# Performance work log

Measured on AMD Instinct MI355X. Metric: run time of the kernel, lower is better.

The kernel has to match this reference:

```python
import jax, jax.numpy as jnp
import numpy as np

K = 5  # adder 'conv' kernel size
PAD = 2  # same padding


def adder2d(x, w):
    """AdderNet L1-distance convolution: out[b,o,i,j] = -sum_{c,kh,kw} |patch - w|.
    x: [B, C, H, W], w: [O, C, K, K] -> [B, O, H, W]
    """
    O = w.shape[0]
    # im2col patches: [B, C*K*K, H, W]
    patches = jax.lax.conv_general_dilated_patches(
        x, (K, K), (1, 1), [(PAD, PAD), (PAD, PAD)])
    wf = w.reshape(O, -1)  # [O, C*K*K]

    def per_out_channel(wo):
        # sequential over O keeps peak memory at one [B, C*K*K, H, W] temp
        return jnp.abs(patches - wo[None, :, None, None]).sum(axis=1)

    out = jax.lax.map(per_out_channel, wf)  # [O, B, H, W]
    return -jnp.transpose(out, (1, 0, 2, 3))


def prelu(x, a):
    # nn.PReLU with a single shared parameter
    return jnp.where(x >= 0, x, a * x)


def maxpool2(x):
    return jax.lax.reduce_window(
        x, -jnp.inf, jax.lax.max,
        window_dimensions=(1, 1, 2, 2), window_strides=(1, 1, 2, 2),
        padding='VALID')


def setup_inputs() -> dict:
    key = jax.random.key(0)
    ks = jax.random.split(key, 8)
    B = 256
    x = jax.random.normal(ks[0], (B, 1, 28, 28), dtype=jnp.float32)
    w1 = jax.random.normal(ks[1], (32, 1, K, K), dtype=jnp.float32) * 0.2
    a1 = jnp.full((1,), 0.25, dtype=jnp.float32)
    w2 = jax.random.normal(ks[2], (32, 32, K, K), dtype=jnp.float32) * 0.07
    a2 = jnp.full((1,), 0.25, dtype=jnp.float32)
    ip1_w = jax.random.normal(ks[3], (2, 32 * 3 * 3), dtype=jnp.float32) * 0.06
    ip1_b = jnp.zeros((2,), dtype=jnp.float32)
    a3 = jnp.full((1,), 0.25, dtype=jnp.float32)
    ip2_w = jax.random.normal(ks[4], (10, 2), dtype=jnp.float32) * 0.7
    return {"x": x, "w1": w1, "a1": a1, "w2": w2, "a2": a2,
            "ip1_w": ip1_w, "ip1_b": ip1_b, "a3": a3, "ip2_w": ip2_w}


def reference(x, w1, a1, w2, a2, ip1_w, ip1_b, a3, ip2_w):
    h = prelu(adder2d(x, w1), a1)          # [B, 32, 28, 28]
    h = prelu(adder2d(h, w2), a2)          # [B, 32, 28, 28]
    h = maxpool2(maxpool2(maxpool2(h)))    # 28 -> 14 -> 7 -> 3
    flat = h.reshape(h.shape[0], -1)       # [B, 288]
    ip1 = prelu(flat @ ip1_w.T + ip1_b, a3)  # [B, 2]
    ip2 = ip1 @ ip2_w.T                    # [B, 10]
    return (ip1, ip2)
```

## Files before the change

kernel.cpp:

```cpp
#include <hip/hip_runtime.h>


__global__ void prep_weights(const float* __restrict__ w1,
                             const float* __restrict__ w2,
                             float* __restrict__ wt1,
                             float* __restrict__ wt2) {
    int tid = threadIdx.x + blockIdx.x * blockDim.x;
    int stride = blockDim.x * gridDim.x;
    for (int i = tid; i < 5 * 5 * 32; i += stride) {
        int o = i & 31, kw = (i >> 5) % 5, kh = i / 160;
        wt1[i] = w1[o * 25 + kh * 5 + kw];
    }
    for (int i = tid; i < 32 * 5 * 5 * 32; i += stride) {
        int o = i & 31, kw = (i >> 5) % 5, kh = ((i >> 5) / 5) % 5, c = i / 800;
        wt2[i] = w2[o * 800 + c * 25 + kh * 5 + kw];
    }
}

__global__ __launch_bounds__(896) void layer1(const float* __restrict__ x,
                                              const float* __restrict__ wt1,
                                              const float* __restrict__ a1v,
                                              float* __restrict__ h1pad) {
    __shared__ float lx[32 * 32];
    const int b = blockIdx.x;
    const int tid = threadIdx.x;

    for (int i = tid; i < 32 * 32; i += 896) {
        int pr = i >> 5, pc = i & 31;
        int r = pr - 2, c = pc - 2;
        float v = 0.f;
        if (r >= 0 && r < 28 && c >= 0 && c < 28) v = x[b * 784 + r * 28 + c];
        lx[i] = v;
    }
    __syncthreads();

    const int o = tid & 31, r = tid >> 5;
    float* orow = h1pad + (size_t)(b * 32 + o) * 784;

    if (r >= 26) {
        float4 z = {0.f, 0.f, 0.f, 0.f};
        float4* dst = (float4*)(orow + (r - 26) * 28);
#pragma unroll
        for (int i = 0; i < 7; i++) dst[i] = z;
        return;
    }

    float wv[25];
    const float* wp = wt1 + o;
#pragma unroll
    for (int k = 0; k < 25; k++) wv[k] = wp[k * 32];

    float acc[26];
#pragma unroll
    for (int j = 0; j < 26; j++) acc[j] = 0.f;

#pragma unroll
    for (int kh = 0; kh < 5; kh++) {
        const float4* xr = (const float4*)&lx[(r + kh) * 32];
        float xw[32];
#pragma unroll
        for (int i = 0; i < 8; i++) {
            float4 v = xr[i];
            xw[4 * i + 0] = v.x; xw[4 * i + 1] = v.y;
            xw[4 * i + 2] = v.z; xw[4 * i + 3] = v.w;
        }
#pragma unroll
        for (int kw = 0; kw < 5; kw++)
#pragma unroll
            for (int j = 0; j < 26; j++)
                acc[j] += fabsf(xw[j + kw] - wv[kh * 5 + kw]);
    }

    const float alpha = a1v[0];
    float outv[28];
    outv[0] = 0.f; outv[1] = 0.f;
#pragma unroll
    for (int j = 0; j < 26; j++) {
        float v = -acc[j];
        outv[j + 2] = (v >= 0.f) ? v : alpha * v;
    }
    float4* dst = (float4*)(orow + (r + 2) * 28);
#pragma unroll
    for (int i = 0; i < 7; i++) {
        float4 v = {outv[4 * i], outv[4 * i + 1], outv[4 * i + 2], outv[4 * i + 3]};
        dst[i] = v;
    }
}

__global__ __launch_bounds__(768, 3) void layer2_conv(
    const float* __restrict__ h1pad, const float* __restrict__ wt2,
    const float* __restrict__ a2v, float* __restrict__ grm) {
    __shared__ float lx[32 * 16 * 28];

    const int bh = blockIdx.x;
    const int b = bh >> 1, half = bh & 1;
    const int tid = threadIdx.x;
    const int r0 = half * 12;

    {
        const float4* src = (const float4*)(h1pad + (size_t)b * 25088 + r0 * 28);
        float4* dst = (float4*)lx;
        for (int i = tid; i < 3584; i += 768) {
            int c = i / 112, rem = i - c * 112;
            dst[c * 112 + rem] = src[c * 196 + rem];
        }
    }
    __syncthreads();

    const int o = tid & 31;
    const int q = tid >> 5;
    const int r = q >> 1;
    const int h = q & 1;
    const int colbase = 12 * h;

    float acc[12];
#pragma unroll
    for (int j = 0; j < 12; j++) acc[j] = 0.f;

    for (int c = 0; c < 32; c++) {
        float wv[25];
        const float* wp = wt2 + c * 800 + o;
#pragma unroll
        for (int k = 0; k < 25; k++) wv[k] = wp[k * 32];

#pragma unroll
        for (int kh = 0; kh < 5; kh++) {
            const float4* xr = (const float4*)&lx[(c * 16 + r + kh) * 28 + colbase];
            float xw[16];
#pragma unroll
            for (int i = 0; i < 4; i++) {
                float4 v = xr[i];
                xw[4 * i + 0] = v.x; xw[4 * i + 1] = v.y;
                xw[4 * i + 2] = v.z; xw[4 * i + 3] = v.w;
            }
#pragma unroll
            for (int kw = 0; kw < 5; kw++)
#pragma unroll
                for (int j = 0; j < 12; j++)
                    acc[j] += fabsf(xw[j + kw] - wv[kh * 5 + kw]);
        }
    }

    const float alpha = a2v[0];
    float p[12];
#pragma unroll
    for (int j = 0; j < 12; j++) {
        float v = -acc[j];
        p[j] = (v >= 0.f) ? v : alpha * v;
    }
    float mFull, mEdge;
    if (h == 0) {
        mFull = p[0]; mEdge = p[8];
#pragma unroll
        for (int j = 1; j < 8; j++) mFull = fmaxf(mFull, p[j]);
#pragma unroll
        for (int j = 9; j < 12; j++) mEdge = fmaxf(mEdge, p[j]);
    } else {
        mEdge = p[0]; mFull = p[4];
#pragma unroll
        for (int j = 1; j < 4; j++) mEdge = fmaxf(mEdge, p[j]);
#pragma unroll
        for (int j = 5; j < 12; j++) mFull = fmaxf(mFull, p[j]);
    }
    float otherEdge = __shfl_xor(mEdge, 32);
    float mMid = fmaxf(mEdge, otherEdge);

    float* g = grm + ((size_t)(b * 2 + half) * 32 + o) * 36 + r * 3;
    if (h == 0) { g[0] = mFull; g[1] = mMid; }
    else        { g[2] = mFull; }
}

__global__ __launch_bounds__(320) void pool_fc(
    const float* __restrict__ grm, const float* __restrict__ ip1_w,
    const float* __restrict__ ip1_b, const float* __restrict__ a3v,
    const float* __restrict__ ip2_w, float* __restrict__ dout) {
    __shared__ float lpool[288];
    const int b = blockIdx.x, t = threadIdx.x;

    if (t < 288) {
        int oo = t / 9, rem = t % 9, ii = rem / 3, jj = rem % 3;
        float m = -1e30f;
#pragma unroll
        for (int k = 0; k < 8; k++) {
            int gr = 8 * ii + k;
            int hf = (gr >= 12) ? 1 : 0;
            int lr = gr - 12 * hf;
            m = fmaxf(m, grm[((size_t)(b * 2 + hf) * 32 + oo) * 36 + lr * 3 + jj]);
        }
        lpool[t] = m;
    }
    __syncthreads();

    if (t < 64) {
        float f0 = 0.f, f1 = 0.f;
        for (int i = t; i < 288; i += 64) {
            float p = lpool[i];
            f0 += p * ip1_w[i];
            f1 += p * ip1_w[288 + i];
        }
#pragma unroll
        for (int off = 32; off > 0; off >>= 1) {
            f0 += __shfl_down(f0, off);
            f1 += __shfl_down(f1, off);
        }
        if (t == 0) {
            float a3 = a3v[0];
            float i0 = f0 + ip1_b[0], i1 = f1 + ip1_b[1];
            i0 = (i0 >= 0.f) ? i0 : a3 * i0;
            i1 = (i1 >= 0.f) ? i1 : a3 * i1;
            dout[b * 2 + 0] = i0;
            dout[b * 2 + 1] = i1;
#pragma unroll
            for (int m = 0; m < 10; m++)
                dout[512 + b * 10 + m] = i0 * ip2_w[m * 2] + i1 * ip2_w[m * 2 + 1];
        }
    }
}

extern "C" void kernel_launch(void* const* d_in, const int* in_sizes, int n_in,
                              void* d_out, int out_size, void* d_ws, size_t ws_size,
                              hipStream_t stream) {
    const float* x     = (const float*)d_in[0];
    const float* w1    = (const float*)d_in[1];
    const float* a1    = (const float*)d_in[2];
    const float* w2    = (const float*)d_in[3];
    const float* a2    = (const float*)d_in[4];
    const float* ip1_w = (const float*)d_in[5];
    const float* ip1_b = (const float*)d_in[6];
    const float* a3    = (const float*)d_in[7];
    const float* ip2_w = (const float*)d_in[8];
    float* out = (float*)d_out;

    char* ws = (char*)d_ws;
    float* wt1   = (float*)(ws);
    float* wt2   = (float*)(ws + 4096);
    float* grm   = (float*)(ws + 131072);
    float* h1pad = (float*)(ws + 4194304);

    prep_weights<<<52, 512, 0, stream>>>(w1, w2, wt1, wt2);
    layer1<<<256, 896, 0, stream>>>(x, wt1, a1, h1pad);
    layer2_conv<<<512, 768, 0, stream>>>(h1pad, wt2, a2, grm);
    pool_fc<<<256, 320, 0, stream>>>(grm, ip1_w, ip1_b, a3, ip2_w, out);
}
```

Baseline: 314.4 us.

## Compute layer-2 adder conv in packed fp16 pairs of input channels

Weights and staged activations for the second adder layer are converted to fp16 and packed two input channels per 32-bit word. The inner loop then uses packed half2 subtract, abs and add, handling two channels per instruction and halving LDS footprint and traffic. Partial sums are flushed to fp32 every 8 channel pairs to limit fp16 accumulation error, though precision loss remains a correctness risk against the fp32 reference.

```diff
diff --git a/kernel.cpp b/kernel.cpp
--- a/kernel.cpp
+++ b/kernel.cpp
@@ -1,19 +1,27 @@
 #include <hip/hip_runtime.h>
-
+#include <hip/hip_fp16.h>
+
+
+typedef unsigned int u32;
+
+__device__ __forceinline__ __half2 bch2(u32 v) { return __builtin_bit_cast(__half2, v); }
+__device__ __forceinline__ u32 bcu(__half2 v) { return __builtin_bit_cast(u32, v); }
 
 __global__ void prep_weights(const float* __restrict__ w1,
                              const float* __restrict__ w2,
                              float* __restrict__ wt1,
-                             float* __restrict__ wt2) {
+                             u32* __restrict__ wt2h) {
     int tid = threadIdx.x + blockIdx.x * blockDim.x;
     int stride = blockDim.x * gridDim.x;
     for (int i = tid; i < 5 * 5 * 32; i += stride) {
         int o = i & 31, kw = (i >> 5) % 5, kh = i / 160;
         wt1[i] = w1[o * 25 + kh * 5 + kw];
     }
-    for (int i = tid; i < 32 * 5 * 5 * 32; i += stride) {
-        int o = i & 31, kw = (i >> 5) % 5, kh = ((i >> 5) / 5) % 5, c = i / 800;
-        wt2[i] = w2[o * 800 + c * 25 + kh * 5 + kw];
+    for (int i = tid; i < 16 * 25 * 32; i += stride) {
+        int o = i & 31, k = (i >> 5) % 25, cp = i / 800;
+        __half lo = __float2half(w2[o * 800 + (2 * cp) * 25 + k]);
+        __half hi = __float2half(w2[o * 800 + (2 * cp + 1) * 25 + k]);
+        wt2h[i] = bcu(__halves2half2(lo, hi));
     }
 }
 
@@ -88,9 +96,9 @@
 }
 
 __global__ __launch_bounds__(768, 3) void layer2_conv(
-    const float* __restrict__ h1pad, const float* __restrict__ wt2,
+    const float* __restrict__ h1pad, const u32* __restrict__ wt2h,
     const float* __restrict__ a2v, float* __restrict__ grm) {
-    __shared__ float lx[32 * 16 * 28];
+    __shared__ u32 lx[16 * 16 * 28];
 
     const int bh = blockIdx.x;
     const int b = bh >> 1, half = bh & 1;
@@ -98,11 +106,22 @@
     const int r0 = half * 12;
 
     {
-        const float4* src = (const float4*)(h1pad + (size_t)b * 25088 + r0 * 28);
-        float4* dst = (float4*)lx;
-        for (int i = tid; i < 3584; i += 768) {
-            int c = i / 112, rem = i - c * 112;
-            dst[c * 112 + rem] = src[c * 196 + rem];
+        const float4* src = (const float4*)h1pad + (size_t)b * 6272 + r0 * 7;
+        uint4* dst = (uint4*)lx;
+        for (int i = tid; i < 1792; i += 768) {
+            int cp = i / 112, rem = i - cp * 112;
+            float4 a = src[cp * 392 + rem];
+            float4 c2 = src[cp * 392 + 196 + rem];
+            auto t0 = __builtin_amdgcn_cvt_pkrtz(a.x, c2.x);
+            auto t1 = __builtin_amdgcn_cvt_pkrtz(a.y, c2.y);
+            auto t2 = __builtin_amdgcn_cvt_pkrtz(a.z, c2.z);
+            auto t3 = __builtin_amdgcn_cvt_pkrtz(a.w, c2.w);
+            uint4 v;
+            v.x = __builtin_bit_cast(u32, t0);
+            v.y = __builtin_bit_cast(u32, t1);
+            v.z = __builtin_bit_cast(u32, t2);
+            v.w = __builtin_bit_cast(u32, t3);
+            dst[cp * 112 + rem] = v;
         }
     }
     __syncthreads();
@@ -113,31 +132,48 @@
     const int h = q & 1;
     const int colbase = 12 * h;
 
-    float acc[12];
-#pragma unroll
-    for (int j = 0; j < 12; j++) acc[j] = 0.f;
-
-    for (int c = 0; c < 32; c++) {
-        float wv[25];
-        const float* wp = wt2 + c * 800 + o;
-#pragma unroll
-        for (int k = 0; k < 25; k++) wv[k] = wp[k * 32];
-
-#pragma unroll
-        for (int kh = 0; kh < 5; kh++) {
-            const float4* xr = (const float4*)&lx[(c * 16 + r + kh) * 28 + colbase];
-            float xw[16];
-#pragma unroll
-            for (int i = 0; i < 4; i++) {
-                float4 v = xr[i];
-                xw[4 * i + 0] = v.x; xw[4 * i + 1] = v.y;
-                xw[4 * i + 2] = v.z; xw[4 * i + 3] = v.w;
+    __half2 accp[12];
+    float facc[12];
+#pragma unroll
+    for (int j = 0; j < 12; j++) {
+        accp[j] = __float2half2_rn(0.f);
+        facc[j] = 0.f;
+    }
+
+    for (int g = 0; g < 2; g++) {
+#pragma unroll 1
+        for (int cp8 = 0; cp8 < 8; cp8++) {
+            const int cp = g * 8 + cp8;
+            u32 wv[25];
+            const u32* wp = wt2h + cp * 800 + o;
+#pragma unroll
+            for (int k = 0; k < 25; k++) wv[k] = wp[k * 32];
+
+#pragma unroll
+            for (int kh = 0; kh < 5; kh++) {
+                const uint4* xr = (const uint4*)&lx[(cp * 16 + r + kh) * 28 + colbase];
+                u32 xw[16];
+#pragma unroll
+                for (int i = 0; i < 4; i++) {
+                    uint4 v = xr[i];
+                    xw[4 * i + 0] = v.x; xw[4 * i + 1] = v.y;
+                    xw[4 * i + 2] = v.z; xw[4 * i + 3] = v.w;
+                }
+#pragma unroll
+                for (int kw = 0; kw < 5; kw++) {
+                    __half2 w = bch2(wv[kh * 5 + kw]);
+#pragma unroll
+                    for (int j = 0; j < 12; j++) {
+                        __half2 xv = bch2(xw[j + kw]);
+                        accp[j] = __hadd2(accp[j], __habs2(__hsub2(xv, w)));
+                    }
+                }
             }
-#pragma unroll
-            for (int kw = 0; kw < 5; kw++)
-#pragma unroll
-                for (int j = 0; j < 12; j++)
-                    acc[j] += fabsf(xw[j + kw] - wv[kh * 5 + kw]);
+        }
+#pragma unroll
+        for (int j = 0; j < 12; j++) {
+            facc[j] += __low2float(accp[j]) + __high2float(accp[j]);
+            accp[j] = __float2half2_rn(0.f);
         }
     }
 
@@ -145,7 +181,7 @@
     float p[12];
 #pragma unroll
     for (int j = 0; j < 12; j++) {
-        float v = -acc[j];
+        float v = -facc[j];
         p[j] = (v >= 0.f) ? v : alpha * v;
     }
     float mFull, mEdge;
@@ -233,12 +269,12 @@
 
     char* ws = (char*)d_ws;
     float* wt1   = (float*)(ws);
-    float* wt2   = (float*)(ws + 4096);
+    u32*   wt2h  = (u32*)(ws + 4096);
     float* grm   = (float*)(ws + 131072);
     float* h1pad = (float*)(ws + 4194304);
 
-    prep_weights<<<52, 512, 0, stream>>>(w1, w2, wt1, wt2);
+    prep_weights<<<52, 512, 0, stream>>>(w1, w2, wt1, wt2h);
     layer1<<<256, 896, 0, stream>>>(x, wt1, a1, h1pad);
-    layer2_conv<<<512, 768, 0, stream>>>(h1pad, wt2, a2, grm);
+    layer2_conv<<<512, 768, 0, stream>>>(h1pad, wt2h, a2, grm);
     pool_fc<<<256, 320, 0, stream>>>(grm, ip1_w, ip1_b, a3, ip2_w, out);
 }
```

After: 253.2 us. 1.24x faster.
